# Optimization experiments

Hardware: AMD Instinct MI355X
Metric: run time of the kernel (lower is better)

## Reference

```python
import jax, jax.numpy as jnp
import numpy as np

# Config mirrors init_kwargs
B = 8            # batch_size
L = 1024         # new tokens per sequence (prefill)
BS = 16          # block_size
MAXB = 128       # max_blocks_per_seq = ceil(2048/16)
H = 8            # num_kv_heads
D = 128          # head_dim
NLAYERS = 2
TOTAL = B * MAXB * NLAYERS  # 2048 total blocks


def setup_inputs() -> dict:
    key = jax.random.key(0)
    k1, k2 = jax.random.split(key)
    return {
        "layer_idx": 0,
        "key_states": jax.random.normal(k1, (B * L, H, D), jnp.float32),
        "value_states": jax.random.normal(k2, (B * L, H, D), jnp.float32),
        "input_len": jnp.full((B,), L, jnp.int32),
        "cu_seqlens": (jnp.arange(B + 1, dtype=jnp.int32) * L),
        "k_cache": jnp.zeros((TOTAL, H, BS, D), jnp.float32),
        "v_cache": jnp.zeros((TOTAL, H, BS, D), jnp.float32),
        "block_tables": jnp.zeros((B, MAXB), jnp.int32),  # layer slice
        "seq_lens": jnp.zeros((B,), jnp.int32),           # layer slice
        "free_blocks": jnp.arange(TOTAL, dtype=jnp.int32),
    }


def reference(layer_idx, key_states, value_states, input_len, cu_seqlens,
              k_cache, v_cache, block_tables, seq_lens, free_blocks):
    # ---- block allocation (vectorized form of the per-sequence python loop) ----
    old_nb = (seq_lens + BS - 1) // BS                 # blocks already held
    new_nb = (seq_lens + input_len + BS - 1) // BS     # blocks needed
    alloc = new_nb - old_nb                            # per-seq new blocks
    cum = jnp.cumsum(alloc)                            # tail-pop order: seq i gets
    num_free = free_blocks.shape[0]                    # free_blocks[num_free-cum[i] : ...]
    start = num_free - cum                             # [B]
    slots = jnp.arange(MAXB, dtype=jnp.int32)[None, :]                  # [1, MAXB]
    valid = (slots >= old_nb[:, None]) & (slots < new_nb[:, None])      # [B, MAXB]
    free_idx = jnp.clip(start[:, None] + (slots - old_nb[:, None]), 0, num_free - 1)
    bt = jnp.where(valid, free_blocks[free_idx], block_tables)          # updated table

    # ---- scatter new K/V tokens into paged cache (store_paged_kv) ----
    # assumes uniform input_len == L (as built in setup_inputs)
    t = jnp.arange(L, dtype=jnp.int32)[None, :]        # [1, L]
    tok_idx = cu_seqlens[:B][:, None] + t              # [B, L] index into packed K/V
    pos = seq_lens[:, None] + t                        # absolute position in sequence
    blk = jnp.take_along_axis(bt, pos // BS, axis=1)   # [B, L] physical block id
    off = pos % BS                                     # [B, L] offset within block

    keys = key_states[tok_idx.ravel()]                 # [B*L, H, D]
    vals = value_states[tok_idx.ravel()]
    k_new = k_cache.at[blk.ravel(), :, off.ravel(), :].set(keys)
    v_new = v_cache.at[blk.ravel(), :, off.ravel(), :].set(vals)
    return jnp.stack([k_new, v_new])  # [2, TOTAL, H, BS, D]
```

## Files before the change

kernel.cpp:

```cpp
#include <hip/hip_runtime.h>

constexpr int B     = 8;
constexpr int L     = 1024;
constexpr int BS    = 16;
constexpr int MAXB  = 128;
constexpr int H     = 8;
constexpr int D     = 128;
constexpr int TOTAL = 2048;
constexpr int CACHE_ELEMS = TOTAL * H * BS * D;

typedef float f4 __attribute__((ext_vector_type(4)));

__global__ void build_inv_kernel(const int* __restrict__ input_len,
                                 const int* __restrict__ block_tables,
                                 const int* __restrict__ seq_lens,
                                 const int* __restrict__ free_blocks,
                                 int* __restrict__ inv) {
    const int tid = threadIdx.x;
    for (int i = tid; i < TOTAL; i += blockDim.x) inv[i] = -1;
    __syncthreads();

    int old_nb[B], new_nb[B], start[B];
    int cum = 0;
    for (int b = 0; b < B; ++b) {
        const int sl = seq_lens[b];
        old_nb[b] = (sl + BS - 1) / BS;
        new_nb[b] = (sl + input_len[b] + BS - 1) / BS;
        cum += new_nb[b] - old_nb[b];
        start[b] = TOTAL - cum;
    }

    for (int b = 0; b < B; ++b) {
        const int j0 = seq_lens[b] / BS;
        for (int j = j0 + tid; j < new_nb[b]; j += blockDim.x) {
            int blk;
            if (j >= old_nb[b]) {
                int fi = start[b] + (j - old_nb[b]);
                fi = min(max(fi, 0), TOTAL - 1);
                blk = free_blocks[fi];
            } else {
                blk = block_tables[b * MAXB + j];
            }
            inv[blk] = (b << 20) | j;
        }
    }
}

__global__ __launch_bounds__(256, 8) void gather_out_kernel(
        const f4* __restrict__ key_states,
        const f4* __restrict__ value_states,
        const f4* __restrict__ k_cache,
        const f4* __restrict__ v_cache,
        const int* __restrict__ input_len,
        const int* __restrict__ cu_seqlens,
        const int* __restrict__ seq_lens,
        const int* __restrict__ inv,
        f4*        __restrict__ out) {
    constexpr int C4   = CACHE_ELEMS / 4;
    constexpr int PB4  = H * BS * D / 4;
    constexpr int CH   = 8;
    constexpr int WG4  = 256 * CH;

    const int base = blockIdx.x * WG4 + threadIdx.x;

    const int c    = base >= C4 ? 1 : 0;
    const int rel0 = base - c * C4;
    const int blk  = rel0 >> 12;

    const f4* __restrict__ cache = c ? v_cache : k_cache;
    const int m = inv[blk];

    f4 vals[CH];
    if (m >= 0) {
        const int b    = m >> 20;
        const int j    = m & 0xFFFFF;
        const int sl   = seq_lens[b];
        const int il   = input_len[b];
        const int tok0 = cu_seqlens[b] - sl;
        const f4* __restrict__ src = c ? value_states : key_states;
        #pragma unroll
        for (int k = 0; k < CH; ++k) {
            const int rel4 = rel0 + k * 256;
            const int r    = rel4 & (PB4 - 1);
            const int h    = r >> 9;
            const int off  = (r >> 5) & 15;
            const int d4   = r & 31;
            const int pos  = j * BS + off;
            if (pos >= sl && pos < sl + il) {
                vals[k] = __builtin_nontemporal_load(
                    &src[(tok0 + pos) * (H * D / 4) + h * 32 + d4]);
            } else {
                vals[k] = __builtin_nontemporal_load(&cache[rel4]);
            }
        }
    } else {
        #pragma unroll
        for (int k = 0; k < CH; ++k)
            vals[k] = __builtin_nontemporal_load(&cache[rel0 + k * 256]);
    }

    #pragma unroll
    for (int k = 0; k < CH; ++k)
        __builtin_nontemporal_store(vals[k], &out[base + k * 256]);
}

extern "C" void kernel_launch(void* const* d_in, const int* in_sizes, int n_in,
                              void* d_out, int out_size, void* d_ws, size_t ws_size,
                              hipStream_t stream) {
    const float* key_states   = (const float*)d_in[1];
    const float* value_states = (const float*)d_in[2];
    const int*   input_len    = (const int*)d_in[3];
    const int*   cu_seqlens   = (const int*)d_in[4];
    const float* k_cache      = (const float*)d_in[5];
    const float* v_cache      = (const float*)d_in[6];
    const int*   block_tables = (const int*)d_in[7];
    const int*   seq_lens     = (const int*)d_in[8];
    const int*   free_blocks  = (const int*)d_in[9];

    int* inv = (int*)d_ws;

    build_inv_kernel<<<1, 256, 0, stream>>>(input_len, block_tables, seq_lens,
                                            free_blocks, inv);

    constexpr int WG4    = 256 * 8;
    const int     total4 = 2 * CACHE_ELEMS / 4;
    const int     blocks = total4 / WG4;
    gather_out_kernel<<<blocks, 256, 0, stream>>>(
        (const f4*)key_states, (const f4*)value_states,
        (const f4*)k_cache, (const f4*)v_cache,
        input_len, cu_seqlens, seq_lens, inv, (f4*)d_out);
}
```

Measured before the change: 463.2 us.

## Make gather kernel persistent with double-buffered chunk loads and branchless source select

The gather kernel now launches a fixed 2048 workgroups, each processing four chunks with two register buffers, so loads of the next chunk are issued before the previous chunk is stored. The per-element source choice becomes a branchless pointer select instead of divergent if/else paths. The aim is more memory-level parallelism per thread and less workgroup launch overhead for a bandwidth-bound copy. The cost is doubled register use, with launch bounds lowered from 8 to 4 waves to match, which reduces occupancy.

```diff
diff --git a/kernel.cpp b/kernel.cpp
--- a/kernel.cpp
+++ b/kernel.cpp
@@ -29,7 +29,6 @@
         cum += new_nb[b] - old_nb[b];
         start[b] = TOTAL - cum;
     }
-
     for (int b = 0; b < B; ++b) {
         const int j0 = seq_lens[b] / BS;
         for (int j = j0 + tid; j < new_nb[b]; j += blockDim.x) {
@@ -46,7 +45,62 @@
     }
 }
 
-__global__ __launch_bounds__(256, 8) void gather_out_kernel(
+constexpr int C4      = CACHE_ELEMS / 4;
+constexpr int PB4     = H * BS * D / 4;
+constexpr int CH      = 8;
+constexpr int CHUNK4  = 256 * CH;
+constexpr int NCHUNK  = 2 * C4 / CHUNK4;
+constexpr int NWG     = 2048;
+constexpr int PER_WG  = NCHUNK / NWG;
+
+__device__ __forceinline__ void load_chunk(
+        int g, int tid,
+        const f4* __restrict__ key_states, const f4* __restrict__ value_states,
+        const f4* __restrict__ k_cache,    const f4* __restrict__ v_cache,
+        const int* __restrict__ input_len, const int* __restrict__ cu_seqlens,
+        const int* __restrict__ seq_lens,  const int* __restrict__ inv,
+        f4 (&vals)[CH]) {
+    const int base = g * CHUNK4 + tid;
+    const int c    = base >= C4 ? 1 : 0;
+    const int rel0 = base - c * C4;
+    const int blk  = rel0 >> 12;
+
+    const f4* __restrict__ cache = c ? v_cache : k_cache;
+    const f4* __restrict__ src   = c ? value_states : key_states;
+
+    const int  m     = inv[blk];
+    const bool fresh = m >= 0;
+    const int  b     = fresh ? (m >> 20) : 0;
+    const int  j     = m & 0xFFFFF;
+    const int  sl    = seq_lens[b];
+    const int  il    = input_len[b];
+    const int  tok0  = cu_seqlens[b] - sl;
+
+    #pragma unroll
+    for (int k = 0; k < CH; ++k) {
+        const int rel4 = rel0 + k * 256;
+        const int r    = rel4 & (PB4 - 1);
+        const int h    = r >> 9;
+        const int off  = (r >> 5) & 15;
+        const int d4   = r & 31;
+        const int pos  = j * BS + off;
+        const bool use_src = fresh & (pos >= sl) & (pos < sl + il);
+        const f4* p = use_src ? (src + ((tok0 + pos) * (H * D / 4) + h * 32 + d4))
+                              : (cache + rel4);
+        vals[k] = __builtin_nontemporal_load(p);
+    }
+}
+
+__device__ __forceinline__ void store_chunk(int g, int tid,
+                                            f4* __restrict__ out,
+                                            const f4 (&vals)[CH]) {
+    const int base = g * CHUNK4 + tid;
+    #pragma unroll
+    for (int k = 0; k < CH; ++k)
+        __builtin_nontemporal_store(vals[k], &out[base + k * 256]);
+}
+
+__global__ __launch_bounds__(256, 4) void gather_out_kernel(
         const f4* __restrict__ key_states,
         const f4* __restrict__ value_states,
         const f4* __restrict__ k_cache,
@@ -56,52 +110,22 @@
         const int* __restrict__ seq_lens,
         const int* __restrict__ inv,
         f4*        __restrict__ out) {
-    constexpr int C4   = CACHE_ELEMS / 4;
-    constexpr int PB4  = H * BS * D / 4;
-    constexpr int CH   = 8;
-    constexpr int WG4  = 256 * CH;
+    const int w   = blockIdx.x;
+    const int tid = threadIdx.x;
 
-    const int base = blockIdx.x * WG4 + threadIdx.x;
-
-    const int c    = base >= C4 ? 1 : 0;
-    const int rel0 = base - c * C4;
-    const int blk  = rel0 >> 12;
-
-    const f4* __restrict__ cache = c ? v_cache : k_cache;
-    const int m = inv[blk];
-
-    f4 vals[CH];
-    if (m >= 0) {
-        const int b    = m >> 20;
-        const int j    = m & 0xFFFFF;
-        const int sl   = seq_lens[b];
-        const int il   = input_len[b];
-        const int tok0 = cu_seqlens[b] - sl;
-        const f4* __restrict__ src = c ? value_states : key_states;
-        #pragma unroll
-        for (int k = 0; k < CH; ++k) {
-            const int rel4 = rel0 + k * 256;
-            const int r    = rel4 & (PB4 - 1);
-            const int h    = r >> 9;
-            const int off  = (r >> 5) & 15;
-            const int d4   = r & 31;
-            const int pos  = j * BS + off;
-            if (pos >= sl && pos < sl + il) {
-                vals[k] = __builtin_nontemporal_load(
-                    &src[(tok0 + pos) * (H * D / 4) + h * 32 + d4]);
-            } else {
-                vals[k] = __builtin_nontemporal_load(&cache[rel4]);
-            }
-        }
-    } else {
-        #pragma unroll
-        for (int k = 0; k < CH; ++k)
-            vals[k] = __builtin_nontemporal_load(&cache[rel0 + k * 256]);
-    }
-
-    #pragma unroll
-    for (int k = 0; k < CH; ++k)
-        __builtin_nontemporal_store(vals[k], &out[base + k * 256]);
+    f4 bufA[CH], bufB[CH];
+    load_chunk(w + 0 * NWG, tid, key_states, value_states, k_cache, v_cache,
+               input_len, cu_seqlens, seq_lens, inv, bufA);
+    load_chunk(w + 1 * NWG, tid, key_states, value_states, k_cache, v_cache,
+               input_len, cu_seqlens, seq_lens, inv, bufB);
+    store_chunk(w + 0 * NWG, tid, out, bufA);
+    load_chunk(w + 2 * NWG, tid, key_states, value_states, k_cache, v_cache,
+               input_len, cu_seqlens, seq_lens, inv, bufA);
+    store_chunk(w + 1 * NWG, tid, out, bufB);
+    load_chunk(w + 3 * NWG, tid, key_states, value_states, k_cache, v_cache,
+               input_len, cu_seqlens, seq_lens, inv, bufB);
+    store_chunk(w + 2 * NWG, tid, out, bufA);
+    store_chunk(w + 3 * NWG, tid, out, bufB);
 }
 
 extern "C" void kernel_launch(void* const* d_in, const int* in_sizes, int n_in,
@@ -122,10 +146,7 @@
     build_inv_kernel<<<1, 256, 0, stream>>>(input_len, block_tables, seq_lens,
                                             free_blocks, inv);
 
-    constexpr int WG4    = 256 * 8;
-    const int     total4 = 2 * CACHE_ELEMS / 4;
-    const int     blocks = total4 / WG4;
-    gather_out_kernel<<<blocks, 256, 0, stream>>>(
+    gather_out_kernel<<<NWG, 256, 0, stream>>>(
         (const f4*)key_states, (const f4*)value_states,
         (const f4*)k_cache, (const f4*)v_cache,
         input_len, cu_seqlens, seq_lens, inv, (f4*)d_out);
```

After: 463.4 us. Within noise of the previous version (+0.0%).

## Fuse block-table inversion into gather kernel, removing separate setup launch

Applied to the files above, without the earlier changes.

Removes the single-workgroup kernel that built an inverse block map in workspace. Each workgroup of the gather kernel now recomputes the allocation itself: it scans all sequences' block slots cooperatively and records the matching (sequence, slot) in shared memory. This drops one kernel launch and the serial dependency on a one-block kernel, in exchange for redundant per-workgroup scanning of about 1024 table entries plus two barriers.

```diff
diff --git a/kernel.cpp b/kernel.cpp
--- a/kernel.cpp
+++ b/kernel.cpp
@@ -11,42 +11,7 @@
 
 typedef float f4 __attribute__((ext_vector_type(4)));
 
-__global__ void build_inv_kernel(const int* __restrict__ input_len,
-                                 const int* __restrict__ block_tables,
-                                 const int* __restrict__ seq_lens,
-                                 const int* __restrict__ free_blocks,
-                                 int* __restrict__ inv) {
-    const int tid = threadIdx.x;
-    for (int i = tid; i < TOTAL; i += blockDim.x) inv[i] = -1;
-    __syncthreads();
-
-    int old_nb[B], new_nb[B], start[B];
-    int cum = 0;
-    for (int b = 0; b < B; ++b) {
-        const int sl = seq_lens[b];
-        old_nb[b] = (sl + BS - 1) / BS;
-        new_nb[b] = (sl + input_len[b] + BS - 1) / BS;
-        cum += new_nb[b] - old_nb[b];
-        start[b] = TOTAL - cum;
-    }
-
-    for (int b = 0; b < B; ++b) {
-        const int j0 = seq_lens[b] / BS;
-        for (int j = j0 + tid; j < new_nb[b]; j += blockDim.x) {
-            int blk;
-            if (j >= old_nb[b]) {
-                int fi = start[b] + (j - old_nb[b]);
-                fi = min(max(fi, 0), TOTAL - 1);
-                blk = free_blocks[fi];
-            } else {
-                blk = block_tables[b * MAXB + j];
-            }
-            inv[blk] = (b << 20) | j;
-        }
-    }
-}
-
-__global__ __launch_bounds__(256, 8) void gather_out_kernel(
+__global__ __launch_bounds__(256, 8) void fused_gather_kernel(
         const f4* __restrict__ key_states,
         const f4* __restrict__ value_states,
         const f4* __restrict__ k_cache,
@@ -54,21 +19,50 @@
         const int* __restrict__ input_len,
         const int* __restrict__ cu_seqlens,
         const int* __restrict__ seq_lens,
-        const int* __restrict__ inv,
+        const int* __restrict__ block_tables,
+        const int* __restrict__ free_blocks,
         f4*        __restrict__ out) {
     constexpr int C4   = CACHE_ELEMS / 4;
     constexpr int PB4  = H * BS * D / 4;
     constexpr int CH   = 8;
     constexpr int WG4  = 256 * CH;
 
-    const int base = blockIdx.x * WG4 + threadIdx.x;
+    const int tid  = threadIdx.x;
+    const int base = blockIdx.x * WG4 + tid;
 
     const int c    = base >= C4 ? 1 : 0;
     const int rel0 = base - c * C4;
     const int blk  = rel0 >> 12;
 
+    __shared__ int sm;
+    if (tid == 0) sm = -1;
+    __syncthreads();
+
+    int cum = 0;
+    #pragma unroll
+    for (int b = 0; b < B; ++b) {
+        const int sl    = seq_lens[b];
+        const int il    = input_len[b];
+        const int oldb  = (sl + BS - 1) / BS;
+        const int newb  = (sl + il + BS - 1) / BS;
+        cum += newb - oldb;
+        const int startb = TOTAL - cum;
+        for (int j = sl / BS + tid; j < newb; j += 256) {
+            int cand;
+            if (j >= oldb) {
+                int fi = startb + (j - oldb);
+                fi = min(max(fi, 0), TOTAL - 1);
+                cand = free_blocks[fi];
+            } else {
+                cand = block_tables[b * MAXB + j];
+            }
+            if (cand == blk) sm = (b << 20) | j;
+        }
+    }
+    __syncthreads();
+    const int m = sm;
+
     const f4* __restrict__ cache = c ? v_cache : k_cache;
-    const int m = inv[blk];
 
     f4 vals[CH];
     if (m >= 0) {
@@ -117,16 +111,12 @@
     const int*   seq_lens     = (const int*)d_in[8];
     const int*   free_blocks  = (const int*)d_in[9];
 
-    int* inv = (int*)d_ws;
-
-    build_inv_kernel<<<1, 256, 0, stream>>>(input_len, block_tables, seq_lens,
-                                            free_blocks, inv);
-
     constexpr int WG4    = 256 * 8;
     const int     total4 = 2 * CACHE_ELEMS / 4;
     const int     blocks = total4 / WG4;
-    gather_out_kernel<<<blocks, 256, 0, stream>>>(
+    fused_gather_kernel<<<blocks, 256, 0, stream>>>(
         (const f4*)key_states, (const f4*)value_states,
         (const f4*)k_cache, (const f4*)v_cache,
-        input_len, cu_seqlens, seq_lens, inv, (f4*)d_out);
+        input_len, cu_seqlens, seq_lens, block_tables, free_blocks,
+        (f4*)d_out);
 }
```

After: 464.5 us. Within noise of the previous version (+0.3%).
